# Kernel tuning notes

Hardware: AMD Instinct MI355X
Metric: run time of the kernel (lower is better)

## Reference

```python
import jax, jax.numpy as jnp
import numpy as np

POOL_SIZE = 4
MAX_DIM = 256
GRID = MAX_DIM // POOL_SIZE  # 64
N_VOX = GRID ** 3            # 262144
N = 1_000_000
C = 64


def setup_inputs() -> dict:
    key = jax.random.key(0)
    k1, k2 = jax.random.split(key)
    vertices = jax.random.randint(k1, (N, 3), 0, MAX_DIM, dtype=jnp.int64)
    features = jax.random.normal(k2, (N, C), dtype=jnp.float32)
    return {"vertices": vertices, "features": features}


def reference(vertices, features):
    # floor-divide coords into voxel grid
    v = vertices // POOL_SIZE                      # [N,3] in [0, GRID)
    vox = v[:, 0] * (GRID * GRID) + v[:, 1] * GRID + v[:, 2]  # [N] flat voxel id
    # amax-pool features per voxel (empty voxels get -inf identity)
    pooled = jax.ops.segment_max(features, vox, num_segments=N_VOX)  # [N_VOX, C]
    # voxels with no points must be 0 (torch output_features initialized to zeros)
    counts = jax.ops.segment_sum(jnp.ones((vertices.shape[0],), jnp.int32), vox,
                                 num_segments=N_VOX)
    out = jnp.where((counts > 0)[:, None], pooled, jnp.zeros((), features.dtype))
    return out.reshape(-1)  # [N_VOX * C]
```

## Files before the change

kernel.cpp:

```cpp
#include <hip/hip_runtime.h>
#include <hip/hip_bf16.h>

#define GRID 64
#define N_VOX (GRID * GRID * GRID)
#define NCH 64


__device__ __forceinline__ int vox_of(int x, int y, int z) {
    return ((x >> 2) << 12) | ((y >> 2) << 6) | (z >> 2);
}

__global__ void k_hist(const int* __restrict__ verts, int* __restrict__ vox,
                       int* __restrict__ counts, int n) {
    int t  = blockIdx.x * blockDim.x + threadIdx.x;
    int p0 = t * 4;
    if (p0 >= n) return;

    if (p0 + 4 <= n) {
        const int4* v4 = (const int4*)verts;
        int4 a = v4[3 * t + 0];
        int4 b = v4[3 * t + 1];
        int4 c = v4[3 * t + 2];
        int w0 = vox_of(a.x, a.y, a.z);
        int w1 = vox_of(a.w, b.x, b.y);
        int w2 = vox_of(b.z, b.w, c.x);
        int w3 = vox_of(c.y, c.z, c.w);
        ((int4*)vox)[t] = make_int4(w0, w1, w2, w3);
        atomicAdd(&counts[w0], 1);
        atomicAdd(&counts[w1], 1);
        atomicAdd(&counts[w2], 1);
        atomicAdd(&counts[w3], 1);
    } else {
        for (int p = p0; p < n; p++) {
            int w = vox_of(verts[3 * p], verts[3 * p + 1], verts[3 * p + 2]);
            vox[p] = w;
            atomicAdd(&counts[w], 1);
        }
    }
}

__global__ void __launch_bounds__(256)
k_bsum(const int* __restrict__ counts, int* __restrict__ bsum) {
    int b = blockIdx.x;
    int t = threadIdx.x;
    int4 c = ((const int4*)counts)[b * 256 + t];
    int s = c.x + c.y + c.z + c.w;
    #pragma unroll
    for (int off = 32; off; off >>= 1) s += __shfl_down(s, off);
    __shared__ int ws[4];
    int lane = t & 63, wid = t >> 6;
    if (lane == 0) ws[wid] = s;
    __syncthreads();
    if (t == 0) bsum[b] = ws[0] + ws[1] + ws[2] + ws[3];
}

__global__ void __launch_bounds__(256) k_scan2(int* __restrict__ bsum) {
    int t = threadIdx.x;
    int v = bsum[t];
    int lane = t & 63;
    int wid  = t >> 6;
    int incl = v;
    #pragma unroll
    for (int off = 1; off < 64; off <<= 1) {
        int u = __shfl_up(incl, off);
        if (lane >= off) incl += u;
    }
    __shared__ int ws[4];
    if (lane == 63) ws[wid] = incl;
    __syncthreads();
    int base = 0;
    for (int i = 0; i < wid; i++) base += ws[i];
    bsum[t] = base + incl - v;
}

__global__ void __launch_bounds__(1024)
k_scanfinal(const int* __restrict__ counts, const int* __restrict__ bsum,
            int2* __restrict__ meta, int* __restrict__ gmut) {
    int g = blockIdx.x * 1024 + threadIdx.x;
    int v = counts[g];
    int lane = threadIdx.x & 63;
    int wid  = threadIdx.x >> 6;

    int incl = v;
    #pragma unroll
    for (int off = 1; off < 64; off <<= 1) {
        int u = __shfl_up(incl, off);
        if (lane >= off) incl += u;
    }
    __shared__ int wsum[16];
    if (lane == 63) wsum[wid] = incl;
    __syncthreads();
    if (wid == 0) {
        int s  = (lane < 16) ? wsum[lane] : 0;
        int si = s;
        #pragma unroll
        for (int off = 1; off < 16; off <<= 1) {
            int u = __shfl_up(si, off);
            if (lane >= off) si += u;
        }
        if (lane < 16) wsum[lane] = si - s;
    }
    __syncthreads();

    int start = bsum[blockIdx.x] + wsum[wid] + incl - v;
    meta[g] = make_int2(start, start + v);
    gmut[g] = start;
}

__global__ void k_scatter_idx(const int* __restrict__ vox,
                              int* __restrict__ gmut,
                              int* __restrict__ sorted_idx, int n) {
    int t  = blockIdx.x * blockDim.x + threadIdx.x;
    int p0 = t * 4;
    if (p0 >= n) return;

    if (p0 + 4 <= n) {
        int4 w = ((const int4*)vox)[t];
        int l0 = atomicAdd(&gmut[w.x], 1);
        int l1 = atomicAdd(&gmut[w.y], 1);
        int l2 = atomicAdd(&gmut[w.z], 1);
        int l3 = atomicAdd(&gmut[w.w], 1);
        sorted_idx[l0] = p0 + 0;
        sorted_idx[l1] = p0 + 1;
        sorted_idx[l2] = p0 + 2;
        sorted_idx[l3] = p0 + 3;
    } else {
        for (int p = p0; p < n; p++) {
            int w = vox[p];
            sorted_idx[atomicAdd(&gmut[w], 1)] = p;
        }
    }
}

__device__ __forceinline__ float4 max4(float4 a, float4 b) {
    float4 r;
    r.x = fmaxf(a.x, b.x); r.y = fmaxf(a.y, b.y);
    r.z = fmaxf(a.z, b.z); r.w = fmaxf(a.w, b.w);
    return r;
}

__global__ void __launch_bounds__(256)
k_gather(const int* __restrict__ sorted_idx,
         const int2* __restrict__ meta,
         const float4* __restrict__ feats4,
         float4* __restrict__ out4) {
    unsigned int t   = blockIdx.x * 256 + threadIdx.x;
    unsigned int vxl = t >> 4;
    unsigned int sub = t & 15;

    int2 se  = meta[vxl];
    int  cnt = se.y - se.x;

    if (cnt == 0) {
        out4[(size_t)vxl * 16 + sub] = make_float4(0.f, 0.f, 0.f, 0.f);
        return;
    }

    int lane  = threadIdx.x & 63;
    int lbase = lane & 48;

    float4 a0 = make_float4(-INFINITY, -INFINITY, -INFINITY, -INFINITY);
    float4 a1 = a0, a2 = a0, a3 = a0;

    for (int base = se.x; base < se.y; base += 16) {
        int nb = min(16, se.y - base);
        int pv = sorted_idx[base + min((int)sub, nb - 1)];
        for (int j = 0; j < nb; j += 4) {
            int p0 = __shfl(pv, lbase + min(j + 0, nb - 1));
            int p1 = __shfl(pv, lbase + min(j + 1, nb - 1));
            int p2 = __shfl(pv, lbase + min(j + 2, nb - 1));
            int p3 = __shfl(pv, lbase + min(j + 3, nb - 1));
            float4 f0 = feats4[(size_t)p0 * 16 + sub];
            float4 f1 = feats4[(size_t)p1 * 16 + sub];
            float4 f2 = feats4[(size_t)p2 * 16 + sub];
            float4 f3 = feats4[(size_t)p3 * 16 + sub];
            a0 = max4(a0, f0);
            a1 = max4(a1, f1);
            a2 = max4(a2, f2);
            a3 = max4(a3, f3);
        }
    }
    out4[(size_t)vxl * 16 + sub] = max4(max4(a0, a1), max4(a2, a3));
}

extern "C" void kernel_launch(void* const* d_in, const int* in_sizes, int n_in,
                              void* d_out, int out_size, void* d_ws, size_t ws_size,
                              hipStream_t stream) {
    const int*   verts = (const int*)d_in[0];
    const float* feats = (const float*)d_in[1];
    float*       out   = (float*)d_out;

    const int n_pts = in_sizes[0] / 3;

    char* w = (char*)d_ws;
    int*  vox        = (int*)w;              w += (size_t)n_pts * 4;
    int*  sorted_idx = (int*)w;              w += (size_t)n_pts * 4;
    int*  counts     = (int*)w;              w += (size_t)N_VOX * 4;
    int2* meta       = (int2*)w;             w += (size_t)N_VOX * 8;
    int*  gmut       = (int*)w;              w += (size_t)N_VOX * 4;
    int*  bsum       = (int*)w;

    hipMemsetAsync(counts, 0, (size_t)N_VOX * 4, stream);

    {
        const int block = 256;
        const int nthr  = (n_pts + 3) / 4;
        const int grid  = (nthr + block - 1) / block;
        k_hist<<<grid, block, 0, stream>>>(verts, vox, counts, n_pts);
    }
    k_bsum<<<256, 256, 0, stream>>>(counts, bsum);
    k_scan2<<<1, 256, 0, stream>>>(bsum);
    k_scanfinal<<<N_VOX / 1024, 1024, 0, stream>>>(counts, bsum, meta, gmut);

    {
        const int block = 256;
        const int nthr  = (n_pts + 3) / 4;
        const int grid  = (nthr + block - 1) / block;
        k_scatter_idx<<<grid, block, 0, stream>>>(vox, gmut, sorted_idx, n_pts);
    }
    {
        const int block = 256;
        const int grid  = (N_VOX * 16) / block;
        k_gather<<<grid, block, 0, stream>>>(sorted_idx, meta,
                                             (const float4*)feats, (float4*)out);
    }
}
```

Baseline: 484.1 us.

## Record atomic ranks in histogram to drop scatter atomics; stage indices in LDS

The histogram kernel now saves the value returned by each atomicAdd as a per-point rank, so the scatter pass computes destinations as start+rank with no second round of atomics. Segment metadata becomes a single start array with a sentinel. The gather kernel loads each block's 16-voxel index span into shared memory when it fits, and uses nontemporal loads and stores for vertices, features and output. This adds a rank buffer write and read and extra shared memory, and features read through nontemporal loads may lose cache reuse.

```diff
diff --git a/kernel.cpp b/kernel.cpp
--- a/kernel.cpp
+++ b/kernel.cpp
@@ -1,40 +1,63 @@
 #include <hip/hip_runtime.h>
-#include <hip/hip_bf16.h>
 
 #define GRID 64
 #define N_VOX (GRID * GRID * GRID)
 #define NCH 64
 
 
+typedef float f32x4 __attribute__((ext_vector_type(4)));
+typedef int   i32x4 __attribute__((ext_vector_type(4)));
+
 __device__ __forceinline__ int vox_of(int x, int y, int z) {
     return ((x >> 2) << 12) | ((y >> 2) << 6) | (z >> 2);
 }
 
+__device__ __forceinline__ float4 max4(float4 a, float4 b) {
+    float4 r;
+    r.x = fmaxf(a.x, b.x); r.y = fmaxf(a.y, b.y);
+    r.z = fmaxf(a.z, b.z); r.w = fmaxf(a.w, b.w);
+    return r;
+}
+
+__device__ __forceinline__ float4 ntload4(const float4* p) {
+    f32x4 v = __builtin_nontemporal_load((const f32x4*)p);
+    return make_float4(v[0], v[1], v[2], v[3]);
+}
+__device__ __forceinline__ void ntstore4(float4* p, float4 v) {
+    f32x4 t; t[0] = v.x; t[1] = v.y; t[2] = v.z; t[3] = v.w;
+    __builtin_nontemporal_store(t, (f32x4*)p);
+}
+__device__ __forceinline__ int4 ntload_i4(const int4* p) {
+    i32x4 v = __builtin_nontemporal_load((const i32x4*)p);
+    return make_int4(v[0], v[1], v[2], v[3]);
+}
+
 __global__ void k_hist(const int* __restrict__ verts, int* __restrict__ vox,
-                       int* __restrict__ counts, int n) {
+                       int* __restrict__ rank, int* __restrict__ counts, int n) {
     int t  = blockIdx.x * blockDim.x + threadIdx.x;
     int p0 = t * 4;
     if (p0 >= n) return;
 
     if (p0 + 4 <= n) {
         const int4* v4 = (const int4*)verts;
-        int4 a = v4[3 * t + 0];
-        int4 b = v4[3 * t + 1];
-        int4 c = v4[3 * t + 2];
+        int4 a = ntload_i4(&v4[3 * t + 0]);
+        int4 b = ntload_i4(&v4[3 * t + 1]);
+        int4 c = ntload_i4(&v4[3 * t + 2]);
         int w0 = vox_of(a.x, a.y, a.z);
         int w1 = vox_of(a.w, b.x, b.y);
         int w2 = vox_of(b.z, b.w, c.x);
         int w3 = vox_of(c.y, c.z, c.w);
         ((int4*)vox)[t] = make_int4(w0, w1, w2, w3);
-        atomicAdd(&counts[w0], 1);
-        atomicAdd(&counts[w1], 1);
-        atomicAdd(&counts[w2], 1);
-        atomicAdd(&counts[w3], 1);
+        int r0 = atomicAdd(&counts[w0], 1);
+        int r1 = atomicAdd(&counts[w1], 1);
+        int r2 = atomicAdd(&counts[w2], 1);
+        int r3 = atomicAdd(&counts[w3], 1);
+        ((int4*)rank)[t] = make_int4(r0, r1, r2, r3);
     } else {
         for (int p = p0; p < n; p++) {
             int w = vox_of(verts[3 * p], verts[3 * p + 1], verts[3 * p + 2]);
-            vox[p] = w;
-            atomicAdd(&counts[w], 1);
+            vox[p]  = w;
+            rank[p] = atomicAdd(&counts[w], 1);
         }
     }
 }
@@ -75,7 +98,7 @@
 
 __global__ void __launch_bounds__(1024)
 k_scanfinal(const int* __restrict__ counts, const int* __restrict__ bsum,
-            int2* __restrict__ meta, int* __restrict__ gmut) {
+            int* __restrict__ gstart) {
     int g = blockIdx.x * 1024 + threadIdx.x;
     int v = counts[g];
     int lane = threadIdx.x & 63;
@@ -103,12 +126,13 @@
     __syncthreads();
 
     int start = bsum[blockIdx.x] + wsum[wid] + incl - v;
-    meta[g] = make_int2(start, start + v);
-    gmut[g] = start;
+    gstart[g] = start;
+    if (g == N_VOX - 1) gstart[N_VOX] = start + v;
 }
 
 __global__ void k_scatter_idx(const int* __restrict__ vox,
-                              int* __restrict__ gmut,
+                              const int* __restrict__ rank,
+                              const int* __restrict__ gstart,
                               int* __restrict__ sorted_idx, int n) {
     int t  = blockIdx.x * blockDim.x + threadIdx.x;
     int p0 = t * 4;
@@ -116,71 +140,78 @@
 
     if (p0 + 4 <= n) {
         int4 w = ((const int4*)vox)[t];
-        int l0 = atomicAdd(&gmut[w.x], 1);
-        int l1 = atomicAdd(&gmut[w.y], 1);
-        int l2 = atomicAdd(&gmut[w.z], 1);
-        int l3 = atomicAdd(&gmut[w.w], 1);
-        sorted_idx[l0] = p0 + 0;
-        sorted_idx[l1] = p0 + 1;
-        sorted_idx[l2] = p0 + 2;
-        sorted_idx[l3] = p0 + 3;
+        int4 r = ((const int4*)rank)[t];
+        sorted_idx[gstart[w.x] + r.x] = p0 + 0;
+        sorted_idx[gstart[w.y] + r.y] = p0 + 1;
+        sorted_idx[gstart[w.z] + r.z] = p0 + 2;
+        sorted_idx[gstart[w.w] + r.w] = p0 + 3;
     } else {
-        for (int p = p0; p < n; p++) {
-            int w = vox[p];
-            sorted_idx[atomicAdd(&gmut[w], 1)] = p;
-        }
-    }
-}
-
-__device__ __forceinline__ float4 max4(float4 a, float4 b) {
-    float4 r;
-    r.x = fmaxf(a.x, b.x); r.y = fmaxf(a.y, b.y);
-    r.z = fmaxf(a.z, b.z); r.w = fmaxf(a.w, b.w);
-    return r;
-}
+        for (int p = p0; p < n; p++)
+            sorted_idx[gstart[vox[p]] + rank[p]] = p;
+    }
+}
+
+#define VPB 16
+#define IDX_CAP 2048
 
 __global__ void __launch_bounds__(256)
 k_gather(const int* __restrict__ sorted_idx,
-         const int2* __restrict__ meta,
+         const int* __restrict__ gstart,
          const float4* __restrict__ feats4,
          float4* __restrict__ out4) {
-    unsigned int t   = blockIdx.x * 256 + threadIdx.x;
-    unsigned int vxl = t >> 4;
-    unsigned int sub = t & 15;
-
-    int2 se  = meta[vxl];
-    int  cnt = se.y - se.x;
+    __shared__ int sst[VPB + 1];
+    __shared__ int sidx[IDX_CAP];
+
+    int vox0 = blockIdx.x * VPB;
+    if (threadIdx.x < VPB + 1) sst[threadIdx.x] = gstart[vox0 + threadIdx.x];
+    __syncthreads();
+
+    int bstart = sst[0];
+    int span   = sst[VPB] - bstart;
+    bool fits  = (span <= IDX_CAP);
+    if (fits) {
+        for (int i = threadIdx.x; i < span; i += 256)
+            sidx[i] = sorted_idx[bstart + i];
+    }
+    __syncthreads();
+
+    int g   = threadIdx.x >> 4;
+    int sub = threadIdx.x & 15;
+    int s0  = sst[g];
+    int cnt = sst[g + 1] - s0;
+    float4* outp = &out4[(size_t)(vox0 + g) * 16 + sub];
 
     if (cnt == 0) {
-        out4[(size_t)vxl * 16 + sub] = make_float4(0.f, 0.f, 0.f, 0.f);
+        ntstore4(outp, make_float4(0.f, 0.f, 0.f, 0.f));
         return;
     }
 
-    int lane  = threadIdx.x & 63;
-    int lbase = lane & 48;
-
+    int off = s0 - bstart;
     float4 a0 = make_float4(-INFINITY, -INFINITY, -INFINITY, -INFINITY);
     float4 a1 = a0, a2 = a0, a3 = a0;
 
-    for (int base = se.x; base < se.y; base += 16) {
-        int nb = min(16, se.y - base);
-        int pv = sorted_idx[base + min((int)sub, nb - 1)];
-        for (int j = 0; j < nb; j += 4) {
-            int p0 = __shfl(pv, lbase + min(j + 0, nb - 1));
-            int p1 = __shfl(pv, lbase + min(j + 1, nb - 1));
-            int p2 = __shfl(pv, lbase + min(j + 2, nb - 1));
-            int p3 = __shfl(pv, lbase + min(j + 3, nb - 1));
-            float4 f0 = feats4[(size_t)p0 * 16 + sub];
-            float4 f1 = feats4[(size_t)p1 * 16 + sub];
-            float4 f2 = feats4[(size_t)p2 * 16 + sub];
-            float4 f3 = feats4[(size_t)p3 * 16 + sub];
-            a0 = max4(a0, f0);
-            a1 = max4(a1, f1);
-            a2 = max4(a2, f2);
-            a3 = max4(a3, f3);
+    for (int j = 0; j < cnt; j += 4) {
+        int j1 = min(j + 1, cnt - 1);
+        int j2 = min(j + 2, cnt - 1);
+        int j3 = min(j + 3, cnt - 1);
+        int p0, p1, p2, p3;
+        if (fits) {
+            p0 = sidx[off + j];  p1 = sidx[off + j1];
+            p2 = sidx[off + j2]; p3 = sidx[off + j3];
+        } else {
+            p0 = sorted_idx[s0 + j];  p1 = sorted_idx[s0 + j1];
+            p2 = sorted_idx[s0 + j2]; p3 = sorted_idx[s0 + j3];
         }
-    }
-    out4[(size_t)vxl * 16 + sub] = max4(max4(a0, a1), max4(a2, a3));
+        float4 f0 = ntload4(&feats4[(size_t)p0 * 16 + sub]);
+        float4 f1 = ntload4(&feats4[(size_t)p1 * 16 + sub]);
+        float4 f2 = ntload4(&feats4[(size_t)p2 * 16 + sub]);
+        float4 f3 = ntload4(&feats4[(size_t)p3 * 16 + sub]);
+        a0 = max4(a0, f0);
+        a1 = max4(a1, f1);
+        a2 = max4(a2, f2);
+        a3 = max4(a3, f3);
+    }
+    ntstore4(outp, max4(max4(a0, a1), max4(a2, a3)));
 }
 
 extern "C" void kernel_launch(void* const* d_in, const int* in_sizes, int n_in,
@@ -194,10 +225,10 @@
 
     char* w = (char*)d_ws;
     int*  vox        = (int*)w;              w += (size_t)n_pts * 4;
+    int*  rank       = (int*)w;              w += (size_t)n_pts * 4;
     int*  sorted_idx = (int*)w;              w += (size_t)n_pts * 4;
     int*  counts     = (int*)w;              w += (size_t)N_VOX * 4;
-    int2* meta       = (int2*)w;             w += (size_t)N_VOX * 8;
-    int*  gmut       = (int*)w;              w += (size_t)N_VOX * 4;
+    int*  gstart     = (int*)w;              w += (size_t)(N_VOX + 16) * 4;
     int*  bsum       = (int*)w;
 
     hipMemsetAsync(counts, 0, (size_t)N_VOX * 4, stream);
@@ -206,22 +237,23 @@
         const int block = 256;
         const int nthr  = (n_pts + 3) / 4;
         const int grid  = (nthr + block - 1) / block;
-        k_hist<<<grid, block, 0, stream>>>(verts, vox, counts, n_pts);
+        k_hist<<<grid, block, 0, stream>>>(verts, vox, rank, counts, n_pts);
     }
     k_bsum<<<256, 256, 0, stream>>>(counts, bsum);
     k_scan2<<<1, 256, 0, stream>>>(bsum);
-    k_scanfinal<<<N_VOX / 1024, 1024, 0, stream>>>(counts, bsum, meta, gmut);
+    k_scanfinal<<<N_VOX / 1024, 1024, 0, stream>>>(counts, bsum, gstart);
 
     {
         const int block = 256;
         const int nthr  = (n_pts + 3) / 4;
         const int grid  = (nthr + block - 1) / block;
-        k_scatter_idx<<<grid, block, 0, stream>>>(vox, gmut, sorted_idx, n_pts);
+        k_scatter_idx<<<grid, block, 0, stream>>>(vox, rank, gstart,
+                                                  sorted_idx, n_pts);
     }
     {
         const int block = 256;
-        const int grid  = (N_VOX * 16) / block;
-        k_gather<<<grid, block, 0, stream>>>(sorted_idx, meta,
+        const int grid  = N_VOX / VPB;
+        k_gather<<<grid, block, 0, stream>>>(sorted_idx, gstart,
                                              (const float4*)feats, (float4*)out);
     }
 }
```

After: 425.3 us. 12.2% less time.
